# Performance work log

Hardware: AMD Instinct MI355X
Metric: run time of the kernel (lower is better)

## Reference

```python
import jax, jax.numpy as jnp
import numpy as np

N, F_IN, HEADS, D_HEAD, HID, OUT, E = 50000, 128, 4, 64, 256, 2, 800000
NEG_SLOPE = 0.2


def setup_inputs() -> dict:
    key = jax.random.key(0)
    ks = jax.random.split(key, 12)
    x = jax.random.normal(ks[0], (N, F_IN), dtype=jnp.float32)
    edge_index = jax.random.randint(ks[1], (2, E), 0, N, dtype=jnp.int64)
    s = 0.05
    W_gat = jax.random.normal(ks[2], (F_IN, HEADS * D_HEAD), dtype=jnp.float32) * s
    att_src = jax.random.normal(ks[3], (HEADS, D_HEAD), dtype=jnp.float32) * s
    att_dst = jax.random.normal(ks[4], (HEADS, D_HEAD), dtype=jnp.float32) * s
    b_gat = jnp.zeros((HEADS * D_HEAD,), dtype=jnp.float32)
    W1 = jax.random.normal(ks[5], (HEADS * D_HEAD, HID), dtype=jnp.float32) * s
    b1 = jnp.zeros((HID,), dtype=jnp.float32)
    W2 = jax.random.normal(ks[6], (HID, HID), dtype=jnp.float32) * s
    b2 = jnp.zeros((HID,), dtype=jnp.float32)
    W3 = jax.random.normal(ks[7], (HID, OUT), dtype=jnp.float32) * s
    b3 = jnp.zeros((OUT,), dtype=jnp.float32)
    return {"x": x, "edge_index": edge_index, "W_gat": W_gat, "att_src": att_src,
            "att_dst": att_dst, "b_gat": b_gat, "W1": W1, "b1": b1,
            "W2": W2, "b2": b2, "W3": W3, "b3": b3}


def _gat(x, edge_index, W_gat, att_src, att_dst, b_gat):
    n = x.shape[0]
    loop = jnp.arange(n, dtype=edge_index.dtype)
    src = jnp.concatenate([edge_index[0], loop])  # [E+N] message sources j
    dst = jnp.concatenate([edge_index[1], loop])  # [E+N] message targets i
    h = (x @ W_gat).reshape(n, HEADS, D_HEAD)      # [N,H,D]
    a_s = jnp.einsum('nhd,hd->nh', h, att_src)     # [N,H]
    a_d = jnp.einsum('nhd,hd->nh', h, att_dst)     # [N,H]
    e = a_s[src] + a_d[dst]                        # [E',H]
    e = jax.nn.leaky_relu(e, NEG_SLOPE)
    # per-destination-node softmax over incoming edges (numerically stable)
    emax = jax.ops.segment_max(e, dst, num_segments=n)
    e = jnp.exp(e - emax[dst])
    denom = jax.ops.segment_sum(e, dst, num_segments=n)
    alpha = e / denom[dst]                         # [E',H]
    msg = h[src] * alpha[:, :, None]               # [E',H,D]
    out = jax.ops.segment_sum(msg, dst, num_segments=n)  # [N,H,D]
    return out.reshape(n, HEADS * D_HEAD) + b_gat


def reference(x, edge_index, W_gat, att_src, att_dst, b_gat, W1, b1, W2, b2, W3, b3):
    h = _gat(x, edge_index, W_gat, att_src, att_dst, b_gat)
    h = jax.nn.relu(h @ W1 + b1)
    h = jax.nn.relu(h @ W2 + b2)
    return h @ W3 + b3
```

## Files before the change

kernel.cpp:

```cpp
#include <hip/hip_runtime.h>
#include <math.h>

#define N_NODES 50000
#define NP 50048
#define F_IN 128
#define HD 256
#define HID 256
#define NE 800000
#define CAP 64
#define NEG_SLOPE 0.2f
#define G1_BLOCKS (NP / 64)

typedef __attribute__((ext_vector_type(8))) __bf16 bf16x8;
typedef __attribute__((ext_vector_type(4))) __bf16 bf16x4;
typedef __attribute__((ext_vector_type(4))) float f32x4;

#define GLD_LDS16(g, l)                                                      \
    __builtin_amdgcn_global_load_lds(                                        \
        (const __attribute__((address_space(1))) unsigned int*)(g),          \
        (__attribute__((address_space(3))) unsigned int*)(l), 16, 0, 0)

#define PB_INIT 196
#define PB_WG   128
#define PB_W1   256
#define PB_W2   256

__global__ __launch_bounds__(256) void prep_kernel(const float* __restrict__ Wg,
                                                   const float* __restrict__ W1,
                                                   const float* __restrict__ W2,
                                                   __bf16* __restrict__ Wg_t,
                                                   __bf16* __restrict__ W1_t,
                                                   __bf16* __restrict__ W2_t,
                                                   int* __restrict__ cnt,
                                                   unsigned short* __restrict__ bucket) {
    int b = blockIdx.x, t = threadIdx.x;
    if (b < PB_INIT) {
        int n = b * 256 + t;
        if (n < N_NODES) { cnt[n] = 1; bucket[n * CAP] = (unsigned short)n; }
    } else if (b < PB_INIT + PB_WG) {
        int i = (b - PB_INIT) * 256 + t;
        int m = i >> 7, k = i & 127;
        Wg_t[i] = (__bf16)Wg[(size_t)k * HD + m];
    } else if (b < PB_INIT + PB_WG + PB_W1) {
        int i = (b - PB_INIT - PB_WG) * 256 + t;
        int m = i >> 8, k = i & 255;
        W1_t[i] = (__bf16)W1[(size_t)k * HID + m];
    } else {
        int i = (b - PB_INIT - PB_WG - PB_W1) * 256 + t;
        int m = i >> 8, k = i & 255;
        W2_t[i] = (__bf16)W2[(size_t)k * HID + m];
    }
}

__global__ __launch_bounds__(256) void g1_fill_kernel(const float* __restrict__ x,
                                                      const __bf16* __restrict__ Bt,
                                                      const float* __restrict__ att_src,
                                                      const float* __restrict__ att_dst,
                                                      const int* __restrict__ ew,
                                                      __bf16* __restrict__ h,
                                                      float* __restrict__ a_s,
                                                      float* __restrict__ a_d,
                                                      int* __restrict__ cnt,
                                                      unsigned short* __restrict__ bucket) {
    __shared__ __bf16 As[64 * 32];
    __shared__ __bf16 Bs[256 * 32];

    if (blockIdx.x >= G1_BLOCKS) {
        int e = (blockIdx.x - G1_BLOCKS) * 256 + threadIdx.x;
        int hi = ew[2 * e + 1];
        unsigned long long bal = __ballot(hi != 0);
        int src, dst;
        if (bal == 0) { src = ew[2 * e]; dst = ew[2 * NE + 2 * e]; }
        else          { src = ew[e];     dst = ew[NE + e]; }
        int pos = atomicAdd(&cnt[dst], 1);
        if (pos < CAP) bucket[dst * CAP + pos] = (unsigned short)src;
        return;
    }

    const int t = threadIdx.x;
    const int lane = t & 63, wv = t >> 6;
    const int lr = lane & 15, q = lane >> 4, lk = q * 8;
    const int col_off = wv * 64;
    const int row0 = blockIdx.x * 64;
    const int sr = t >> 2, sk = (t & 3) * 8;
    const int arow = row0 + sr;
    const bool avalid = arow < N_NODES;

    f32x4 acc[4][4];
#pragma unroll
    for (int r = 0; r < 4; ++r)
#pragma unroll
        for (int c = 0; c < 4; ++c) acc[r][c] = f32x4{0.f, 0.f, 0.f, 0.f};

    for (int k0 = 0; k0 < F_IN; k0 += 32) {
        float4 v0 = {0, 0, 0, 0}, v1 = {0, 0, 0, 0};
        if (avalid) {
            const float* xp = &x[(size_t)arow * F_IN + k0 + sk];
            v0 = *(const float4*)xp;
            v1 = *(const float4*)(xp + 4);
        }
        bf16x8 o;
        o[0] = (__bf16)v0.x; o[1] = (__bf16)v0.y; o[2] = (__bf16)v0.z; o[3] = (__bf16)v0.w;
        o[4] = (__bf16)v1.x; o[5] = (__bf16)v1.y; o[6] = (__bf16)v1.z; o[7] = (__bf16)v1.w;
        *(bf16x8*)&As[sr * 32 + sk] = o;
#pragma unroll
        for (int s = 0; s < 4; ++s) {
            int r = s * 64 + sr;
            GLD_LDS16(&Bt[(size_t)r * F_IN + k0 + sk], &Bs[r * 32 + sk]);
        }
        __syncthreads();
        bf16x8 af[4], bfr[4];
#pragma unroll
        for (int i = 0; i < 4; ++i) {
            af[i]  = *(const bf16x8*)&As[(i * 16 + lr) * 32 + lk];
            bfr[i] = *(const bf16x8*)&Bs[(col_off + i * 16 + lr) * 32 + lk];
        }
#pragma unroll
        for (int r = 0; r < 4; ++r)
#pragma unroll
            for (int c = 0; c < 4; ++c)
                acc[r][c] = __builtin_amdgcn_mfma_f32_16x16x32_bf16(af[r], bfr[c], acc[r][c], 0, 0, 0);
        __syncthreads();
    }

    float asv[4], adv[4];
#pragma unroll
    for (int c = 0; c < 4; ++c) {
        int col = col_off + c * 16 + lr;
        asv[c] = att_src[col];
        adv[c] = att_dst[col];
    }
    float ps[4][4], pd[4][4];
#pragma unroll
    for (int r = 0; r < 4; ++r)
#pragma unroll
        for (int i = 0; i < 4; ++i) { ps[r][i] = 0.f; pd[r][i] = 0.f; }

#pragma unroll
    for (int c = 0; c < 4; ++c) {
        int col = col_off + c * 16 + lr;
#pragma unroll
        for (int r = 0; r < 4; ++r) {
#pragma unroll
            for (int i = 0; i < 4; ++i) {
                int row = row0 + r * 16 + q * 4 + i;
                float v = acc[r][c][i];
                h[(size_t)row * HD + col] = (__bf16)v;
                ps[r][i] += v * asv[c];
                pd[r][i] += v * adv[c];
            }
        }
    }
#pragma unroll
    for (int r = 0; r < 4; ++r)
#pragma unroll
        for (int i = 0; i < 4; ++i) {
#pragma unroll
            for (int m = 1; m < 16; m <<= 1) {
                ps[r][i] += __shfl_xor(ps[r][i], m);
                pd[r][i] += __shfl_xor(pd[r][i], m);
            }
        }
    if (lr == 0) {
#pragma unroll
        for (int r = 0; r < 4; ++r)
#pragma unroll
            for (int i = 0; i < 4; ++i) {
                int row = row0 + r * 16 + q * 4 + i;
                a_s[row * 4 + wv] = ps[r][i];
                a_d[row * 4 + wv] = pd[r][i];
            }
    }
}

__device__ __forceinline__ float lrelu(float v) { return v >= 0.f ? v : NEG_SLOPE * v; }

__global__ __launch_bounds__(64) void gat_aggregate_kernel(const __bf16* __restrict__ h,
                                                           const float* __restrict__ a_s,
                                                           const float* __restrict__ a_d,
                                                           const int* __restrict__ cnt,
                                                           const unsigned short* __restrict__ bucket,
                                                           const float* __restrict__ b_gat,
                                                           __bf16* __restrict__ gat) {
    __shared__ unsigned short s_src[64];
    __shared__ float s_alpha[64][4];
    const int lane = threadIdx.x;
    const int n = blockIdx.x;

    int deg = cnt[n];
    if (deg > CAP) deg = CAP;
    int src = n;
    float4 e = {-1e30f, -1e30f, -1e30f, -1e30f};
    float4 ad = *(const float4*)&a_d[n * 4];
    if (lane < deg) {
        src = bucket[n * CAP + lane];
        float4 as4 = *(const float4*)&a_s[src * 4];
        e.x = lrelu(as4.x + ad.x);
        e.y = lrelu(as4.y + ad.y);
        e.z = lrelu(as4.z + ad.z);
        e.w = lrelu(as4.w + ad.w);
    }
    float4 m = e;
#pragma unroll
    for (int off = 1; off < 64; off <<= 1) {
        m.x = fmaxf(m.x, __shfl_xor(m.x, off));
        m.y = fmaxf(m.y, __shfl_xor(m.y, off));
        m.z = fmaxf(m.z, __shfl_xor(m.z, off));
        m.w = fmaxf(m.w, __shfl_xor(m.w, off));
    }
    float4 wgt = {0, 0, 0, 0};
    if (lane < deg) {
        wgt.x = __expf(e.x - m.x); wgt.y = __expf(e.y - m.y);
        wgt.z = __expf(e.z - m.z); wgt.w = __expf(e.w - m.w);
    }
    float4 s = wgt;
#pragma unroll
    for (int off = 1; off < 64; off <<= 1) {
        s.x += __shfl_xor(s.x, off); s.y += __shfl_xor(s.y, off);
        s.z += __shfl_xor(s.z, off); s.w += __shfl_xor(s.w, off);
    }
    s_src[lane] = (unsigned short)src;
    s_alpha[lane][0] = wgt.x / s.x;
    s_alpha[lane][1] = wgt.y / s.y;
    s_alpha[lane][2] = wgt.z / s.z;
    s_alpha[lane][3] = wgt.w / s.w;
    __syncthreads();

    const int half = lane >> 5;
    const int l32 = lane & 31;
    const int c0 = l32 * 8;
    const int head = l32 >> 3;
    float acc[8];
#pragma unroll
    for (int k = 0; k < 8; ++k) acc[k] = 0.f;

    const int mde = (deg + 1) & ~1;
    int j = 0;
    for (; j + 8 <= mde; j += 8) {
        int j0 = j + half, j1 = j + 2 + half, j2 = j + 4 + half, j3 = j + 6 + half;
        int s0 = s_src[j0], s1 = s_src[j1], s2 = s_src[j2], s3 = s_src[j3];
        float a0 = s_alpha[j0][head], a1 = s_alpha[j1][head];
        float a2 = s_alpha[j2][head], a3 = s_alpha[j3][head];
        bf16x8 h0 = *(const bf16x8*)&h[(size_t)s0 * HD + c0];
        bf16x8 h1 = *(const bf16x8*)&h[(size_t)s1 * HD + c0];
        bf16x8 h2 = *(const bf16x8*)&h[(size_t)s2 * HD + c0];
        bf16x8 h3 = *(const bf16x8*)&h[(size_t)s3 * HD + c0];
#pragma unroll
        for (int k = 0; k < 8; ++k)
            acc[k] += a0 * (float)h0[k] + a1 * (float)h1[k]
                    + a2 * (float)h2[k] + a3 * (float)h3[k];
    }
    for (; j < mde; j += 2) {
        int j0 = j + half;
        int s0 = s_src[j0];
        float a0 = s_alpha[j0][head];
        bf16x8 h0 = *(const bf16x8*)&h[(size_t)s0 * HD + c0];
#pragma unroll
        for (int k = 0; k < 8; ++k)
            acc[k] += a0 * (float)h0[k];
    }
#pragma unroll
    for (int k = 0; k < 8; ++k) acc[k] += __shfl_xor(acc[k], 32);

    if (half == 0) {
        float4 bg0 = *(const float4*)&b_gat[c0];
        float4 bg1 = *(const float4*)&b_gat[c0 + 4];
        bf16x8 o;
        o[0] = (__bf16)(acc[0] + bg0.x); o[1] = (__bf16)(acc[1] + bg0.y);
        o[2] = (__bf16)(acc[2] + bg0.z); o[3] = (__bf16)(acc[3] + bg0.w);
        o[4] = (__bf16)(acc[4] + bg1.x); o[5] = (__bf16)(acc[5] + bg1.y);
        o[6] = (__bf16)(acc[6] + bg1.z); o[7] = (__bf16)(acc[7] + bg1.w);
        *(bf16x8*)&gat[(size_t)n * HD + c0] = o;
    }
}

__global__ __launch_bounds__(256) void fused_mlp_kernel(const __bf16* __restrict__ A,
                                                        const __bf16* __restrict__ W1t,
                                                        const __bf16* __restrict__ W2t,
                                                        const float* __restrict__ b1,
                                                        const float* __restrict__ b2,
                                                        const float* __restrict__ W3,
                                                        const float* __restrict__ b3,
                                                        float* __restrict__ out) {
    __shared__ __bf16 As[64 * 32];
    __shared__ __bf16 Ws[256 * 32];
    __shared__ __bf16 h1s[8 * 64 * 32];
    __shared__ float s_out[64][2];
    const int t = threadIdx.x;
    const int lane = t & 63, wv = t >> 6;
    const int lr = lane & 15, q = lane >> 4, lk = q * 8;
    const int col_off = wv * 64;
    const int row0 = blockIdx.x * 64;
    const int sr = t >> 2, sk = (t & 3) * 8;

    if (t < 128) ((float*)s_out)[t] = 0.f;

    f32x4 acc[4][4];
#pragma unroll
    for (int r = 0; r < 4; ++r)
#pragma unroll
        for (int c = 0; c < 4; ++c) acc[r][c] = f32x4{0.f, 0.f, 0.f, 0.f};

    for (int k0 = 0; k0 < HD; k0 += 32) {
        GLD_LDS16(&A[(size_t)(row0 + sr) * HD + k0 + sk], &As[sr * 32 + sk]);
#pragma unroll
        for (int s = 0; s < 4; ++s) {
            int r = s * 64 + sr;
            GLD_LDS16(&W1t[(size_t)r * HD + k0 + sk], &Ws[r * 32 + sk]);
        }
        __syncthreads();
        bf16x8 af[4], bfr[4];
#pragma unroll
        for (int i = 0; i < 4; ++i) {
            af[i]  = *(const bf16x8*)&As[(i * 16 + lr) * 32 + lk];
            bfr[i] = *(const bf16x8*)&Ws[(col_off + i * 16 + lr) * 32 + lk];
        }
#pragma unroll
        for (int r = 0; r < 4; ++r)
#pragma unroll
            for (int c = 0; c < 4; ++c)
                acc[r][c] = __builtin_amdgcn_mfma_f32_16x16x32_bf16(af[r], bfr[c], acc[r][c], 0, 0, 0);
        __syncthreads();
    }
#pragma unroll
    for (int c = 0; c < 4; ++c) {
        int col = col_off + c * 16 + lr;
        float bv = b1[col];
        int cb = (col >> 5) * 2048;
        int kk = col & 31;
#pragma unroll
        for (int r = 0; r < 4; ++r)
#pragma unroll
            for (int i = 0; i < 4; ++i) {
                int row = r * 16 + q * 4 + i;
                float v = fmaxf(acc[r][c][i] + bv, 0.f);
                h1s[cb + row * 32 + kk] = (__bf16)v;
                acc[r][c][i] = 0.f;
            }
    }
    __syncthreads();

    for (int k0 = 0; k0 < HID; k0 += 32) {
#pragma unroll
        for (int s = 0; s < 4; ++s) {
            int r = s * 64 + sr;
            GLD_LDS16(&W2t[(size_t)r * HID + k0 + sk], &Ws[r * 32 + sk]);
        }
        __syncthreads();
        const int cb = (k0 >> 5) * 2048;
        bf16x8 af[4], bfr[4];
#pragma unroll
        for (int i = 0; i < 4; ++i) {
            af[i]  = *(const bf16x8*)&h1s[cb + (i * 16 + lr) * 32 + lk];
            bfr[i] = *(const bf16x8*)&Ws[(col_off + i * 16 + lr) * 32 + lk];
        }
#pragma unroll
        for (int r = 0; r < 4; ++r)
#pragma unroll
            for (int c = 0; c < 4; ++c)
                acc[r][c] = __builtin_amdgcn_mfma_f32_16x16x32_bf16(af[r], bfr[c], acc[r][c], 0, 0, 0);
        __syncthreads();
    }

    float b2v[4], w30[4], w31[4];
#pragma unroll
    for (int c = 0; c < 4; ++c) {
        int col = col_off + c * 16 + lr;
        b2v[c] = b2[col];
        w30[c] = W3[col * 2];
        w31[c] = W3[col * 2 + 1];
    }
#pragma unroll
    for (int r = 0; r < 4; ++r) {
#pragma unroll
        for (int i = 0; i < 4; ++i) {
            float o0 = 0.f, o1 = 0.f;
#pragma unroll
            for (int c = 0; c < 4; ++c) {
                float v = fmaxf(acc[r][c][i] + b2v[c], 0.f);
                o0 += v * w30[c];
                o1 += v * w31[c];
            }
#pragma unroll
            for (int m = 1; m < 16; m <<= 1) {
                o0 += __shfl_xor(o0, m);
                o1 += __shfl_xor(o1, m);
            }
            if (lr == 0) {
                int row = r * 16 + q * 4 + i;
                atomicAdd(&s_out[row][0], o0);
                atomicAdd(&s_out[row][1], o1);
            }
        }
    }
    __syncthreads();
    if (t < 128) {
        int row = t >> 1, o = t & 1;
        int g = row0 + row;
        if (g < N_NODES) out[g * 2 + o] = s_out[row][o] + b3[o];
    }
}

extern "C" void kernel_launch(void* const* d_in, const int* in_sizes, int n_in,
                              void* d_out, int out_size, void* d_ws, size_t ws_size,
                              hipStream_t stream) {
    const float* x       = (const float*)d_in[0];
    const int*   ei      = (const int*)d_in[1];
    const float* W_gat   = (const float*)d_in[2];
    const float* att_src = (const float*)d_in[3];
    const float* att_dst = (const float*)d_in[4];
    const float* b_gat   = (const float*)d_in[5];
    const float* W1      = (const float*)d_in[6];
    const float* b1      = (const float*)d_in[7];
    const float* W2      = (const float*)d_in[8];
    const float* b2      = (const float*)d_in[9];
    const float* W3      = (const float*)d_in[10];
    const float* b3      = (const float*)d_in[11];
    float* out = (float*)d_out;

    char* ws = (char*)d_ws;
    __bf16* h_bf   = (__bf16*)ws;  ws += (size_t)NP * HD * 2;
    __bf16* gat_bf = (__bf16*)ws;  ws += (size_t)NP * HD * 2;
    __bf16* Wg_t   = (__bf16*)ws;  ws += (size_t)HD * F_IN * 2;
    __bf16* W1_t   = (__bf16*)ws;  ws += (size_t)HID * HD * 2;
    __bf16* W2_t   = (__bf16*)ws;  ws += (size_t)HID * HID * 2;
    float* a_s     = (float*)ws;   ws += (size_t)NP * 4 * 4;
    float* a_d     = (float*)ws;   ws += (size_t)NP * 4 * 4;
    int* cnt       = (int*)ws;     ws += (size_t)N_NODES * 4;
    unsigned short* bucket = (unsigned short*)ws;
    ws += (size_t)N_NODES * CAP * 2;

    prep_kernel<<<PB_INIT + PB_WG + PB_W1 + PB_W2, 256, 0, stream>>>(
        W_gat, W1, W2, Wg_t, W1_t, W2_t, cnt, bucket);
    g1_fill_kernel<<<G1_BLOCKS + NE / 256, 256, 0, stream>>>(
        x, Wg_t, att_src, att_dst, ei, h_bf, a_s, a_d, cnt, bucket);
    gat_aggregate_kernel<<<N_NODES, 64, 0, stream>>>(h_bf, a_s, a_d, cnt, bucket,
                                                     b_gat, gat_bf);
    fused_mlp_kernel<<<NP / 64, 256, 0, stream>>>(gat_bf, W1_t, W2_t, b1, b2, W3, b3, out);
}
```

Measured before the change: 240.5 us.

## Batch edge fill per thread, pad degree counters, prefetch first h rows

The edge-bucket fill path now handles 8 edges per thread, using 64-bit loads and issuing all atomics before the bucket stores, so more memory operations are in flight. Degree counters are spaced 4 ints apart to reduce atomic contention on shared cache lines. The aggregate kernel prefetches the first four neighbour feature rows via shuffles before the softmax reductions, hiding their latency behind the softmax math. The cost is more registers, fewer fill blocks, and a larger counter buffer.

```diff
diff --git a/kernel.cpp b/kernel.cpp
--- a/kernel.cpp
+++ b/kernel.cpp
@@ -10,6 +10,9 @@
 #define CAP 64
 #define NEG_SLOPE 0.2f
 #define G1_BLOCKS (NP / 64)
+#define FILL_ILP 8
+#define FILL_BLOCKS ((NE + 256 * FILL_ILP - 1) / (256 * FILL_ILP))
+#define CNT_STRIDE 4
 
 typedef __attribute__((ext_vector_type(8))) __bf16 bf16x8;
 typedef __attribute__((ext_vector_type(4))) __bf16 bf16x4;
@@ -36,7 +39,7 @@
     int b = blockIdx.x, t = threadIdx.x;
     if (b < PB_INIT) {
         int n = b * 256 + t;
-        if (n < N_NODES) { cnt[n] = 1; bucket[n * CAP] = (unsigned short)n; }
+        if (n < N_NODES) { cnt[(size_t)n * CNT_STRIDE] = 1; bucket[n * CAP] = (unsigned short)n; }
     } else if (b < PB_INIT + PB_WG) {
         int i = (b - PB_INIT) * 256 + t;
         int m = i >> 7, k = i & 127;
@@ -66,14 +69,44 @@
     __shared__ __bf16 Bs[256 * 32];
 
     if (blockIdx.x >= G1_BLOCKS) {
-        int e = (blockIdx.x - G1_BLOCKS) * 256 + threadIdx.x;
-        int hi = ew[2 * e + 1];
-        unsigned long long bal = __ballot(hi != 0);
-        int src, dst;
-        if (bal == 0) { src = ew[2 * e]; dst = ew[2 * NE + 2 * e]; }
-        else          { src = ew[e];     dst = ew[NE + e]; }
-        int pos = atomicAdd(&cnt[dst], 1);
-        if (pos < CAP) bucket[dst * CAP + pos] = (unsigned short)src;
+        const int base = (blockIdx.x - G1_BLOCKS) * (256 * FILL_ILP) + threadIdx.x;
+        long long p[FILL_ILP];
+        bool v[FILL_ILP];
+        int s[FILL_ILP], d[FILL_ILP], pos[FILL_ILP];
+        int hiall = 0;
+#pragma unroll
+        for (int k = 0; k < FILL_ILP; ++k) {
+            const int e = base + k * 256;
+            v[k] = e < NE;
+            p[k] = 0;
+            if (v[k]) p[k] = *(const long long*)&ew[2 * e];
+            hiall |= (int)(p[k] >> 32);
+        }
+        unsigned long long bal = __ballot(hiall != 0);
+        if (bal == 0) {
+#pragma unroll
+            for (int k = 0; k < FILL_ILP; ++k) {
+                const int e = base + k * 256;
+                s[k] = (int)p[k];
+                d[k] = 0;
+                if (v[k]) d[k] = ew[2 * NE + 2 * e];
+            }
+        } else {
+#pragma unroll
+            for (int k = 0; k < FILL_ILP; ++k) {
+                const int e = base + k * 256;
+                s[k] = 0; d[k] = 0;
+                if (v[k]) { s[k] = ew[e]; d[k] = ew[NE + e]; }
+            }
+        }
+#pragma unroll
+        for (int k = 0; k < FILL_ILP; ++k) {
+            pos[k] = CAP;
+            if (v[k]) pos[k] = atomicAdd(&cnt[(size_t)d[k] * CNT_STRIDE], 1);
+        }
+#pragma unroll
+        for (int k = 0; k < FILL_ILP; ++k)
+            if (pos[k] < CAP) bucket[d[k] * CAP + pos[k]] = (unsigned short)s[k];
         return;
     }
 
@@ -187,14 +220,31 @@
     const int lane = threadIdx.x;
     const int n = blockIdx.x;
 
-    int deg = cnt[n];
+    int deg = cnt[(size_t)n * CNT_STRIDE];
     if (deg > CAP) deg = CAP;
     int src = n;
-    float4 e = {-1e30f, -1e30f, -1e30f, -1e30f};
     float4 ad = *(const float4*)&a_d[n * 4];
+    float4 as4 = {0, 0, 0, 0};
     if (lane < deg) {
         src = bucket[n * CAP + lane];
-        float4 as4 = *(const float4*)&a_s[src * 4];
+        as4 = *(const float4*)&a_s[src * 4];
+    }
+
+    const int half = lane >> 5;
+    const int l32 = lane & 31;
+    const int c0 = l32 * 8;
+    const int head = l32 >> 3;
+    const int pj0 = __shfl(src, half);
+    const int pj1 = __shfl(src, 2 + half);
+    const int pj2 = __shfl(src, 4 + half);
+    const int pj3 = __shfl(src, 6 + half);
+    const bf16x8 hp0 = *(const bf16x8*)&h[(size_t)pj0 * HD + c0];
+    const bf16x8 hp1 = *(const bf16x8*)&h[(size_t)pj1 * HD + c0];
+    const bf16x8 hp2 = *(const bf16x8*)&h[(size_t)pj2 * HD + c0];
+    const bf16x8 hp3 = *(const bf16x8*)&h[(size_t)pj3 * HD + c0];
+
+    float4 e = {-1e30f, -1e30f, -1e30f, -1e30f};
+    if (lane < deg) {
         e.x = lrelu(as4.x + ad.x);
         e.y = lrelu(as4.y + ad.y);
         e.z = lrelu(as4.z + ad.z);
@@ -226,29 +276,36 @@
     s_alpha[lane][3] = wgt.w / s.w;
     __syncthreads();
 
-    const int half = lane >> 5;
-    const int l32 = lane & 31;
-    const int c0 = l32 * 8;
-    const int head = l32 >> 3;
     float acc[8];
 #pragma unroll
     for (int k = 0; k < 8; ++k) acc[k] = 0.f;
 
     const int mde = (deg + 1) & ~1;
     int j = 0;
-    for (; j + 8 <= mde; j += 8) {
-        int j0 = j + half, j1 = j + 2 + half, j2 = j + 4 + half, j3 = j + 6 + half;
-        int s0 = s_src[j0], s1 = s_src[j1], s2 = s_src[j2], s3 = s_src[j3];
-        float a0 = s_alpha[j0][head], a1 = s_alpha[j1][head];
-        float a2 = s_alpha[j2][head], a3 = s_alpha[j3][head];
-        bf16x8 h0 = *(const bf16x8*)&h[(size_t)s0 * HD + c0];
-        bf16x8 h1 = *(const bf16x8*)&h[(size_t)s1 * HD + c0];
-        bf16x8 h2 = *(const bf16x8*)&h[(size_t)s2 * HD + c0];
-        bf16x8 h3 = *(const bf16x8*)&h[(size_t)s3 * HD + c0];
+    if (mde >= 8) {
+        const float a0 = s_alpha[half][head];
+        const float a1 = s_alpha[2 + half][head];
+        const float a2 = s_alpha[4 + half][head];
+        const float a3 = s_alpha[6 + half][head];
 #pragma unroll
         for (int k = 0; k < 8; ++k)
-            acc[k] += a0 * (float)h0[k] + a1 * (float)h1[k]
-                    + a2 * (float)h2[k] + a3 * (float)h3[k];
+            acc[k] += a0 * (float)hp0[k] + a1 * (float)hp1[k]
+                    + a2 * (float)hp2[k] + a3 * (float)hp3[k];
+        j = 8;
+        for (; j + 8 <= mde; j += 8) {
+            int j0 = j + half, j1 = j + 2 + half, j2 = j + 4 + half, j3 = j + 6 + half;
+            int s0 = s_src[j0], s1 = s_src[j1], s2 = s_src[j2], s3 = s_src[j3];
+            float b0 = s_alpha[j0][head], b1 = s_alpha[j1][head];
+            float b2 = s_alpha[j2][head], b3 = s_alpha[j3][head];
+            bf16x8 h0 = *(const bf16x8*)&h[(size_t)s0 * HD + c0];
+            bf16x8 h1 = *(const bf16x8*)&h[(size_t)s1 * HD + c0];
+            bf16x8 h2 = *(const bf16x8*)&h[(size_t)s2 * HD + c0];
+            bf16x8 h3 = *(const bf16x8*)&h[(size_t)s3 * HD + c0];
+#pragma unroll
+            for (int k = 0; k < 8; ++k)
+                acc[k] += b0 * (float)h0[k] + b1 * (float)h1[k]
+                        + b2 * (float)h2[k] + b3 * (float)h3[k];
+        }
     }
     for (; j < mde; j += 2) {
         int j0 = j + half;
@@ -426,13 +483,13 @@
     __bf16* W2_t   = (__bf16*)ws;  ws += (size_t)HID * HID * 2;
     float* a_s     = (float*)ws;   ws += (size_t)NP * 4 * 4;
     float* a_d     = (float*)ws;   ws += (size_t)NP * 4 * 4;
-    int* cnt       = (int*)ws;     ws += (size_t)N_NODES * 4;
+    int* cnt       = (int*)ws;     ws += (size_t)N_NODES * CNT_STRIDE * 4;
     unsigned short* bucket = (unsigned short*)ws;
     ws += (size_t)N_NODES * CAP * 2;
 
     prep_kernel<<<PB_INIT + PB_WG + PB_W1 + PB_W2, 256, 0, stream>>>(
         W_gat, W1, W2, Wg_t, W1_t, W2_t, cnt, bucket);
-    g1_fill_kernel<<<G1_BLOCKS + NE / 256, 256, 0, stream>>>(
+    g1_fill_kernel<<<G1_BLOCKS + FILL_BLOCKS, 256, 0, stream>>>(
         x, Wg_t, att_src, att_dst, ei, h_bf, a_s, a_d, cnt, bucket);
     gat_aggregate_kernel<<<N_NODES, 64, 0, stream>>>(h_bf, a_s, a_d, cnt, bucket,
                                                      b_gat, gat_bf);
```

Result: slower. 245.8 us (+2.2%).
